# Kernel tuning notes

Measured on AMD Instinct MI355X. Metric: run time of the kernel, lower is better.

Reference implementation:

```python
import jax, jax.numpy as jnp
import numpy as np

# Production-scale dims (see shape_source)
B, H, W, C = 8, 64, 64, 256
KH, KW = 3, 3
BASES = 16
FILTERS = 256


def setup_inputs() -> dict:
    key = jax.random.key(0)
    k1, k2, k3, k4 = jax.random.split(key, 4)
    x = jax.random.normal(k1, (B, H, W, C), dtype=jnp.float32)
    # P: channel-mixing matrix [C, C] (initialized to identity in build, then assigned)
    P = jax.random.normal(k2, (C, C), dtype=jnp.float32) * 0.05
    # Q: per-channel basis kernels [C, kh, kw, bases]
    Q = jax.random.normal(k3, (C, KH, KW, BASES), dtype=jnp.float32) * 0.1
    # S: basis-combination weights [C, bases, filters]
    S = jax.random.normal(k4, (C, BASES, FILTERS), dtype=jnp.float32) * 0.05
    return {"x": x, "P": P, "Q": Q, "S": S}


def reference(x, P, Q, S):
    # --- Step 1: channel mixing (the vectorized_map over calculate_J) ---
    # J[o] = sum_c x[..., c] * P[o, c]  ->  one GEMM over channels
    mixed = jnp.einsum('bhwc,oc->bhwo', x, P)  # [B,H,W,C]

    C_ = P.shape[0]
    kh, kw, bases = Q.shape[1], Q.shape[2], Q.shape[3]

    # --- Step 2: per-channel conv with `bases` basis kernels (the map_fn loop) ---
    # Expressed as ONE grouped (depthwise-style) conv: group c produces outputs
    # [c*bases : (c+1)*bases], matching kernel flatten order (c, b).
    rhs = jnp.transpose(Q, (1, 2, 0, 3)).reshape(kh, kw, 1, C_ * bases)  # HWIO
    dw = jax.lax.conv_general_dilated(
        mixed, rhs, window_strides=(1, 1), padding='VALID',
        dimension_numbers=('NHWC', 'HWIO', 'NHWC'),
        feature_group_count=C_,
    )  # [B, H-kh+1, W-kw+1, C*bases], channel index k = c*bases + b

    b, h, w, _ = dw.shape
    # tau in the original: [B, h, w, bases, C]
    tau = dw.reshape(b, h, w, C_, bases).transpose(0, 1, 2, 4, 3)

    # --- Step 3: basis-weighted combination (the vectorized_map over calculate_O) ---
    # Original flattens tau row-major over (bases, C) and S[:, :, f] row-major over
    # (C, bases), then does an elementwise dot over the flat axis. Replicate exactly.
    Tflat = tau.reshape(b, h, w, bases * C_)          # flat index k = b_idx*C + c
    Sflat = S.reshape(C_ * bases, S.shape[-1])        # flat index k = c*bases + b_idx
    O = jnp.einsum('bhwk,kf->bhwf', Tflat, Sflat)     # [B, h, w, filters]
    return O
```

## Files before the change

### kernel.cpp

```cpp
#include <hip/hip_runtime.h>
#include <hip/hip_bf16.h>

typedef __attribute__((ext_vector_type(4))) float f32x4;
typedef __attribute__((ext_vector_type(8))) short bf16x8;

#define M_TOT 30752

__device__ __forceinline__ unsigned short f2bf(float f) {
  unsigned int u = __float_as_uint(f);
  u = u + 0x7FFF + ((u >> 16) & 1);
  return (unsigned short)(u >> 16);
}

__device__ __forceinline__ void gload16(const void* g, void* l) {
  __builtin_amdgcn_global_load_lds((const __attribute__((address_space(1))) unsigned int*)g,
                                   (__attribute__((address_space(3))) unsigned int*)l,
                                   16, 0, 0);
}

__global__ __launch_bounds__(256) void prep1(const float* __restrict__ x,
                                             const float* __restrict__ Q,
                                             const float* __restrict__ S,
                                             unsigned short* __restrict__ xb,
                                             float* __restrict__ Keff) {
  const int bid = blockIdx.x;
  const int t = threadIdx.x;

  if (bid < 4096) {
    int i = bid * 256 + t;
    const f32x4* xp = (const f32x4*)x;
    f32x4 a = xp[2 * i];
    f32x4 b = xp[2 * i + 1];
    bf16x8 o;
    o[0] = (short)f2bf(a[0]); o[1] = (short)f2bf(a[1]);
    o[2] = (short)f2bf(a[2]); o[3] = (short)f2bf(a[3]);
    o[4] = (short)f2bf(b[0]); o[5] = (short)f2bf(b[1]);
    o[6] = (short)f2bf(b[2]); o[7] = (short)f2bf(b[3]);
    ((bf16x8*)xb)[i] = o;
    return;
  }

  const int bid2 = bid - 4096;
  const int o = bid2 / 9;
  const int kk = bid2 - o * 9;
  const int f = t;
  const int qb = o * 144 + kk * 16;
  const int sb = (o >> 4) * 4096 + (o & 15) * 256 + f;
  float acc = 0.f;
#pragma unroll
  for (int bi = 0; bi < 16; ++bi)
    acc = fmaf(Q[qb + bi], S[sb + bi * 65536], acc);
  Keff[bid2 * 256 + f] = acc;
}

__global__ __launch_bounds__(256) void k2t_k(const float* __restrict__ P,
                                             const float* __restrict__ Keff,
                                             unsigned short* __restrict__ K2t) {
  const int kk = blockIdx.x >> 6;
  const int f0 = (blockIdx.x & 63) * 4;
  const int ci = threadIdx.x;
  float acc[4] = {0.f, 0.f, 0.f, 0.f};
#pragma unroll 8
  for (int o = 0; o < 256; ++o) {
    float pv = P[o * 256 + ci];
    const float* ke = Keff + (o * 9 + kk) * 256 + f0;
    acc[0] = fmaf(pv, ke[0], acc[0]);
    acc[1] = fmaf(pv, ke[1], acc[1]);
    acc[2] = fmaf(pv, ke[2], acc[2]);
    acc[3] = fmaf(pv, ke[3], acc[3]);
  }
#pragma unroll
  for (int j = 0; j < 4; ++j)
    K2t[kk * 65536 + (f0 + j) * 256 + ci] = f2bf(acc[j]);
}

__global__ __launch_bounds__(512) void conv_gemm(const unsigned short* __restrict__ xb,
                                                 const unsigned short* __restrict__ K2t,
                                                 float* __restrict__ out) {
  __shared__ unsigned short A0[128 * 64];
  __shared__ unsigned short A1[128 * 64];
  __shared__ unsigned short A2[128 * 64];
  __shared__ unsigned short B0[256 * 64];
  __shared__ unsigned short B1[256 * 64];
  __shared__ unsigned short B2[256 * 64];

  const int tid = threadIdx.x;
  const int lane = tid & 63;
  const int wm = (tid >> 6) >> 2;
  const int wn = (tid >> 6) & 3;
  const int m0 = blockIdx.x * 128;

  const int swslot = ((tid & 7) ^ ((tid >> 3) & 7)) * 8;
  const int rA = tid >> 3;

  int gA0, gA1;
  {
    int m = m0 + rA; if (m >= M_TOT) m = M_TOT - 1;
    int b = m / 3844; int rem = m - b * 3844;
    int h = rem / 62; int w = rem - h * 62;
    gA0 = ((b * 64 + h) * 64 + w) * 256 + swslot;
    m = m0 + rA + 64; if (m >= M_TOT) m = M_TOT - 1;
    b = m / 3844; rem = m - b * 3844;
    h = rem / 62; w = rem - h * 62;
    gA1 = ((b * 64 + h) * 64 + w) * 256 + swslot;
  }

  f32x4 zero = {0.f, 0.f, 0.f, 0.f};
  f32x4 acc[4][4];
#pragma unroll
  for (int i = 0; i < 4; ++i)
#pragma unroll
    for (int j = 0; j < 4; ++j) acc[i][j] = zero;

  const int rl = lane & 15;
  const int kg = lane >> 4;
  const int xm = (lane & 7) << 4;

#define STAGE_A(t, bufA)                                                       \
  {                                                                            \
    int kk_ = (t) >> 2, cb_ = (t) & 3;                                         \
    int kh_ = kk_ / 3, kw_ = kk_ - kh_ * 3;                                    \
    int offA_ = kh_ * 16384 + kw_ * 256 + cb_ * 64;                            \
    gload16(xb + gA0 + offA_, &bufA[tid * 8]);                                 \
    gload16(xb + gA1 + offA_, &bufA[(tid + 512) * 8]);                         \
  }

#define STAGE_B(t, bufB)                                                       \
  {                                                                            \
    int kk_ = (t) >> 2, cb_ = (t) & 3;                                         \
    int offB_ = kk_ * 65536 + cb_ * 64 + swslot;                               \
    _Pragma("unroll")                                                          \
    for (int q = 0; q < 4; ++q)                                                \
      gload16(K2t + offB_ + (rA + 64 * q) * 256, &bufB[(tid + 512 * q) * 8]);  \
  }

#define PHASE(ks, bufA, bufB, STAGE_STMT)                                      \
  {                                                                            \
    bf16x8 af[4], bfr[4];                                                      \
    int cbyte = ((ks) * 64 + kg * 16) ^ xm;                                    \
    _Pragma("unroll")                                                          \
    for (int mi = 0; mi < 4; ++mi)                                             \
      af[mi] = *(const bf16x8*)((const char*)bufA + (wm * 64 + mi * 16 + rl) * 128 + cbyte); \
    _Pragma("unroll")                                                          \
    for (int ni = 0; ni < 4; ++ni)                                             \
      bfr[ni] = *(const bf16x8*)((const char*)bufB + (wn * 64 + ni * 16 + rl) * 128 + cbyte); \
    STAGE_STMT;                                                                \
    asm volatile("s_waitcnt lgkmcnt(0)" ::: "memory");                         \
    __builtin_amdgcn_sched_barrier(0);                                         \
    __builtin_amdgcn_s_setprio(1);                                             \
    _Pragma("unroll")                                                          \
    for (int mi = 0; mi < 4; ++mi)                                             \
      _Pragma("unroll")                                                        \
      for (int ni = 0; ni < 4; ++ni)                                           \
        acc[mi][ni] = __builtin_amdgcn_mfma_f32_16x16x32_bf16(                 \
            af[mi], bfr[ni], acc[mi][ni], 0, 0, 0);                            \
    __builtin_amdgcn_s_setprio(0);                                             \
  }

#define STEP(t, cA, cB, nA, nB)                                                \
  {                                                                            \
    if ((t) == 35) asm volatile("s_waitcnt vmcnt(0)" ::: "memory");            \
    else           asm volatile("s_waitcnt vmcnt(6)" ::: "memory");            \
    __builtin_amdgcn_sched_barrier(0);                                         \
    __builtin_amdgcn_s_barrier();                                              \
    __builtin_amdgcn_sched_barrier(0);                                         \
    PHASE(0, cA, cB, { if ((t) + 2 < 36) STAGE_A((t) + 2, nA); })              \
    __builtin_amdgcn_sched_barrier(0);                                         \
    __builtin_amdgcn_s_barrier();                                              \
    __builtin_amdgcn_sched_barrier(0);                                         \
    PHASE(1, cA, cB, { if ((t) + 2 < 36) STAGE_B((t) + 2, nB); })              \
  }

  STAGE_A(0, A0); STAGE_B(0, B0);
  STAGE_A(1, A1); STAGE_B(1, B1);

  for (int tt = 0; tt < 12; ++tt) {
    int t0 = tt * 3;
    STEP(t0,     A0, B0, A2, B2);
    STEP(t0 + 1, A1, B1, A0, B0);
    STEP(t0 + 2, A2, B2, A1, B1);
  }

#pragma unroll
  for (int mi = 0; mi < 4; ++mi) {
    int mb = m0 + wm * 64 + mi * 16 + kg * 4;
#pragma unroll
    for (int ni = 0; ni < 4; ++ni) {
      int f = wn * 64 + ni * 16 + rl;
#pragma unroll
      for (int r = 0; r < 4; ++r) {
        int m = mb + r;
        if (m < M_TOT) out[m * 256 + f] = acc[mi][ni][r];
      }
    }
  }
#undef STAGE_A
#undef STAGE_B
#undef PHASE
#undef STEP
}

extern "C" void kernel_launch(void* const* d_in, const int* in_sizes, int n_in,
                              void* d_out, int out_size, void* d_ws, size_t ws_size,
                              hipStream_t stream) {
  const float* x = (const float*)d_in[0];
  const float* P = (const float*)d_in[1];
  const float* Q = (const float*)d_in[2];
  const float* S = (const float*)d_in[3];
  float* out = (float*)d_out;

  char* ws = (char*)d_ws;
  unsigned short* xb   = (unsigned short*)ws;
  unsigned short* K2t  = (unsigned short*)(ws + 16777216);
  float*          Keff = (float*)(ws + 16777216 + 1179648);

  prep1<<<4096 + 2304, 256, 0, stream>>>(x, Q, S, xb, Keff);
  k2t_k<<<576, 256, 0, stream>>>(P, Keff, K2t);
  conv_gemm<<<241, 512, 0, stream>>>(xb, K2t, out);
}
```

Baseline: 80.27 us.

## Split-K across warp halves in conv GEMM with LDS reduction; reuse S loads in prep

The conv GEMM now splits each 64-wide K chunk between two groups of 4 waves. Each wave computes a full 128-row by 64-column tile (8x4 MFMAs) over half of K, and the two halves are reduced through LDS at the end. The per-K-step two-phase barrier structure collapses into one phase per step. LDS staging is reworked into a single 144KB buffer without the XOR swizzle, which risks bank conflicts, and accumulator registers double. The Keff prep kernel loads the 16 S values once per channel and reuses them across all 9 taps, cutting its block count from 2304 to 256.

Result: faster. 77.76 us (-3.1%).

```diff
diff --git a/kernel.cpp b/kernel.cpp
--- a/kernel.cpp
+++ b/kernel.cpp
@@ -40,17 +40,19 @@
     return;
   }
 
-  const int bid2 = bid - 4096;
-  const int o = bid2 / 9;
-  const int kk = bid2 - o * 9;
-  const int f = t;
-  const int qb = o * 144 + kk * 16;
-  const int sb = (o >> 4) * 4096 + (o & 15) * 256 + f;
-  float acc = 0.f;
-#pragma unroll
-  for (int bi = 0; bi < 16; ++bi)
-    acc = fmaf(Q[qb + bi], S[sb + bi * 65536], acc);
-  Keff[bid2 * 256 + f] = acc;
+  const int o = bid - 4096;
+  float s[16];
+  const float* sp = S + (o >> 4) * 4096 + (o & 15) * 256 + t;
+#pragma unroll
+  for (int bi = 0; bi < 16; ++bi) s[bi] = sp[bi * 65536];
+  const float* qp = Q + o * 144;
+#pragma unroll
+  for (int kk = 0; kk < 9; ++kk) {
+    float a = 0.f;
+#pragma unroll
+    for (int bi = 0; bi < 16; ++bi) a = fmaf(qp[kk * 16 + bi], s[bi], a);
+    Keff[(o * 9 + kk) * 256 + t] = a;
+  }
 }
 
 __global__ __launch_bounds__(256) void k2t_k(const float* __restrict__ P,
@@ -74,87 +76,59 @@
     K2t[kk * 65536 + (f0 + j) * 256 + ci] = f2bf(acc[j]);
 }
 
-__global__ __launch_bounds__(512) void conv_gemm(const unsigned short* __restrict__ xb,
-                                                 const unsigned short* __restrict__ K2t,
-                                                 float* __restrict__ out) {
-  __shared__ unsigned short A0[128 * 64];
-  __shared__ unsigned short A1[128 * 64];
-  __shared__ unsigned short A2[128 * 64];
-  __shared__ unsigned short B0[256 * 64];
-  __shared__ unsigned short B1[256 * 64];
-  __shared__ unsigned short B2[256 * 64];
+__global__ __launch_bounds__(512, 2) void conv_gemm(const unsigned short* __restrict__ xb,
+                                                    const unsigned short* __restrict__ K2t,
+                                                    float* __restrict__ out) {
+  __shared__ __attribute__((aligned(16))) char smem[147456];
+  unsigned short* const A0 = (unsigned short*)(smem);
+  unsigned short* const B0 = (unsigned short*)(smem + 16384);
+  unsigned short* const A1 = (unsigned short*)(smem + 49152);
+  unsigned short* const B1 = (unsigned short*)(smem + 65536);
+  unsigned short* const A2 = (unsigned short*)(smem + 98304);
+  unsigned short* const B2 = (unsigned short*)(smem + 114688);
+  float* const red = (float*)smem;
 
   const int tid = threadIdx.x;
   const int lane = tid & 63;
-  const int wm = (tid >> 6) >> 2;
+  const int sk = tid >> 8;
   const int wn = (tid >> 6) & 3;
   const int m0 = blockIdx.x * 128;
 
-  const int swslot = ((tid & 7) ^ ((tid >> 3) & 7)) * 8;
-  const int rA = tid >> 3;
-
-  int gA0, gA1;
+  const int rl = lane & 15;
+  const int kg = lane >> 4;
+
+  int gAa;
   {
-    int m = m0 + rA; if (m >= M_TOT) m = M_TOT - 1;
+    int m = m0 + (tid >> 2); if (m >= M_TOT) m = M_TOT - 1;
     int b = m / 3844; int rem = m - b * 3844;
     int h = rem / 62; int w = rem - h * 62;
-    gA0 = ((b * 64 + h) * 64 + w) * 256 + swslot;
-    m = m0 + rA + 64; if (m >= M_TOT) m = M_TOT - 1;
-    b = m / 3844; rem = m - b * 3844;
-    h = rem / 62; w = rem - h * 62;
-    gA1 = ((b * 64 + h) * 64 + w) * 256 + swslot;
-  }
+    gAa = ((b * 64 + h) * 64 + w) * 256 + (tid & 3) * 8;
+  }
+  const int fB0 = (tid >> 2) * 256 + (tid & 3) * 8;
+  const int fB1 = ((tid >> 2) + 128) * 256 + (tid & 3) * 8;
 
   f32x4 zero = {0.f, 0.f, 0.f, 0.f};
-  f32x4 acc[4][4];
-#pragma unroll
-  for (int i = 0; i < 4; ++i)
+  f32x4 acc[8][4];
+#pragma unroll
+  for (int i = 0; i < 8; ++i)
 #pragma unroll
     for (int j = 0; j < 4; ++j) acc[i][j] = zero;
 
-  const int rl = lane & 15;
-  const int kg = lane >> 4;
-  const int xm = (lane & 7) << 4;
-
-#define STAGE_A(t, bufA)                                                       \
+  const int aoff = sk * 8192 + rl * 64 + kg * 16;
+  const int boff = sk * 16384 + (wn * 64 + rl) * 64 + kg * 16;
+
+#define STAGE(t, bufA, bufB)                                                   \
   {                                                                            \
     int kk_ = (t) >> 2, cb_ = (t) & 3;                                         \
     int kh_ = kk_ / 3, kw_ = kk_ - kh_ * 3;                                    \
     int offA_ = kh_ * 16384 + kw_ * 256 + cb_ * 64;                            \
-    gload16(xb + gA0 + offA_, &bufA[tid * 8]);                                 \
-    gload16(xb + gA1 + offA_, &bufA[(tid + 512) * 8]);                         \
-  }
-
-#define STAGE_B(t, bufB)                                                       \
-  {                                                                            \
-    int kk_ = (t) >> 2, cb_ = (t) & 3;                                         \
-    int offB_ = kk_ * 65536 + cb_ * 64 + swslot;                               \
-    _Pragma("unroll")                                                          \
-    for (int q = 0; q < 4; ++q)                                                \
-      gload16(K2t + offB_ + (rA + 64 * q) * 256, &bufB[(tid + 512 * q) * 8]);  \
-  }
-
-#define PHASE(ks, bufA, bufB, STAGE_STMT)                                      \
-  {                                                                            \
-    bf16x8 af[4], bfr[4];                                                      \
-    int cbyte = ((ks) * 64 + kg * 16) ^ xm;                                    \
-    _Pragma("unroll")                                                          \
-    for (int mi = 0; mi < 4; ++mi)                                             \
-      af[mi] = *(const bf16x8*)((const char*)bufA + (wm * 64 + mi * 16 + rl) * 128 + cbyte); \
-    _Pragma("unroll")                                                          \
-    for (int ni = 0; ni < 4; ++ni)                                             \
-      bfr[ni] = *(const bf16x8*)((const char*)bufB + (wn * 64 + ni * 16 + rl) * 128 + cbyte); \
-    STAGE_STMT;                                                                \
-    asm volatile("s_waitcnt lgkmcnt(0)" ::: "memory");                         \
-    __builtin_amdgcn_sched_barrier(0);                                         \
-    __builtin_amdgcn_s_setprio(1);                                             \
-    _Pragma("unroll")                                                          \
-    for (int mi = 0; mi < 4; ++mi)                                             \
-      _Pragma("unroll")                                                        \
-      for (int ni = 0; ni < 4; ++ni)                                           \
-        acc[mi][ni] = __builtin_amdgcn_mfma_f32_16x16x32_bf16(                 \
-            af[mi], bfr[ni], acc[mi][ni], 0, 0, 0);                            \
-    __builtin_amdgcn_s_setprio(0);                                             \
+    int offB_ = kk_ * 65536 + cb_ * 64;                                        \
+    gload16(xb + gAa + offA_,       &bufA[tid * 8]);                           \
+    gload16(xb + gAa + offA_ + 32,  &bufA[(tid + 512) * 8]);                   \
+    gload16(K2t + offB_ + fB0,      &bufB[tid * 8]);                           \
+    gload16(K2t + offB_ + fB1,      &bufB[(tid + 512) * 8]);                   \
+    gload16(K2t + offB_ + fB0 + 32, &bufB[(tid + 1024) * 8]);                  \
+    gload16(K2t + offB_ + fB1 + 32, &bufB[(tid + 1536) * 8]);                  \
   }
 
 #define STEP(t, cA, cB, nA, nB)                                                \
@@ -164,15 +138,28 @@
     __builtin_amdgcn_sched_barrier(0);                                         \
     __builtin_amdgcn_s_barrier();                                              \
     __builtin_amdgcn_sched_barrier(0);                                         \
-    PHASE(0, cA, cB, { if ((t) + 2 < 36) STAGE_A((t) + 2, nA); })              \
+    bf16x8 af[8], bfr[4];                                                      \
+    _Pragma("unroll")                                                          \
+    for (int mi = 0; mi < 8; ++mi)                                             \
+      af[mi] = *(const bf16x8*)((const char*)(cA) + aoff + mi * 1024);         \
+    _Pragma("unroll")                                                          \
+    for (int ni = 0; ni < 4; ++ni)                                             \
+      bfr[ni] = *(const bf16x8*)((const char*)(cB) + boff + ni * 1024);        \
+    if ((t) < 34) { STAGE((t) + 2, nA, nB); }                                  \
+    asm volatile("s_waitcnt lgkmcnt(0)" ::: "memory");                         \
     __builtin_amdgcn_sched_barrier(0);                                         \
-    __builtin_amdgcn_s_barrier();                                              \
-    __builtin_amdgcn_sched_barrier(0);                                         \
-    PHASE(1, cA, cB, { if ((t) + 2 < 36) STAGE_B((t) + 2, nB); })              \
-  }
-
-  STAGE_A(0, A0); STAGE_B(0, B0);
-  STAGE_A(1, A1); STAGE_B(1, B1);
+    __builtin_amdgcn_s_setprio(1);                                             \
+    _Pragma("unroll")                                                          \
+    for (int mi = 0; mi < 8; ++mi)                                             \
+      _Pragma("unroll")                                                        \
+      for (int ni = 0; ni < 4; ++ni)                                           \
+        acc[mi][ni] = __builtin_amdgcn_mfma_f32_16x16x32_bf16(                 \
+            af[mi], bfr[ni], acc[mi][ni], 0, 0, 0);                            \
+    __builtin_amdgcn_s_setprio(0);                                             \
+  }
+
+  STAGE(0, A0, B0);
+  STAGE(1, A1, B1);
 
   for (int tt = 0; tt < 12; ++tt) {
     int t0 = tt * 3;
@@ -181,22 +168,40 @@
     STEP(t0 + 2, A2, B2, A1, B1);
   }
 
-#pragma unroll
-  for (int mi = 0; mi < 4; ++mi) {
-    int mb = m0 + wm * 64 + mi * 16 + kg * 4;
-#pragma unroll
-    for (int ni = 0; ni < 4; ++ni) {
-      int f = wn * 64 + ni * 16 + rl;
-#pragma unroll
-      for (int r = 0; r < 4; ++r) {
-        int m = mb + r;
-        if (m < M_TOT) out[m * 256 + f] = acc[mi][ni][r];
+  __syncthreads();
+
+#pragma unroll
+  for (int round = 0; round < 2; ++round) {
+    if (sk == 1) {
+#pragma unroll
+      for (int mc = 0; mc < 4; ++mc)
+#pragma unroll
+        for (int ni = 0; ni < 4; ++ni)
+          *(f32x4*)((char*)red + (((wn * 4 + mc) * 4 + ni) * 64 + lane) * 16) =
+              acc[round * 4 + mc][ni];
+    }
+    __syncthreads();
+    if (sk == 0) {
+#pragma unroll
+      for (int mc = 0; mc < 4; ++mc) {
+        int mi = round * 4 + mc;
+        int mb = m0 + mi * 16 + kg * 4;
+#pragma unroll
+        for (int ni = 0; ni < 4; ++ni) {
+          f32x4 o = *(f32x4*)((char*)red + (((wn * 4 + mc) * 4 + ni) * 64 + lane) * 16);
+          o += acc[mi][ni];
+          int f = wn * 64 + ni * 16 + rl;
+#pragma unroll
+          for (int r = 0; r < 4; ++r) {
+            int m = mb + r;
+            if (m < M_TOT) out[m * 256 + f] = o[r];
+          }
+        }
       }
     }
-  }
-#undef STAGE_A
-#undef STAGE_B
-#undef PHASE
+    __syncthreads();
+  }
+#undef STAGE
 #undef STEP
 }
 
@@ -214,7 +219,7 @@
   unsigned short* K2t  = (unsigned short*)(ws + 16777216);
   float*          Keff = (float*)(ws + 16777216 + 1179648);
 
-  prep1<<<4096 + 2304, 256, 0, stream>>>(x, Q, S, xb, Keff);
+  prep1<<<4096 + 256, 256, 0, stream>>>(x, Q, S, xb, Keff);
   k2t_k<<<576, 256, 0, stream>>>(P, Keff, K2t);
   conv_gemm<<<241, 512, 0, stream>>>(xb, K2t, out);
 }
```

## Fuse weight-prep kernels and split GEMM phases into finer MFMA/load interleave

Applied to the files above, without the earlier changes.

Merges the Keff and K2t preparation into a single kernel that launches alongside the x-to-bf16 conversion. Each block recomputes its Keff slice into LDS, so the Keff round trip through global memory and one launch are gone, at the cost of some redundant Q·S work. The conv GEMM now keeps A and B in one contiguous LDS buffer per stage. Each K step is split into four 8-MFMA chunks with the B prefetch spread across them, aiming to overlap global loads with compute more evenly. The price is extra barriers per step.

After: 77.92 us. 2.9% less time.

```diff
diff --git a/kernel.cpp b/kernel.cpp
--- a/kernel.cpp
+++ b/kernel.cpp
@@ -18,16 +18,18 @@
                                    16, 0, 0);
 }
 
-__global__ __launch_bounds__(256) void prep1(const float* __restrict__ x,
-                                             const float* __restrict__ Q,
-                                             const float* __restrict__ S,
-                                             unsigned short* __restrict__ xb,
-                                             float* __restrict__ Keff) {
+__global__ __launch_bounds__(256) void fused_k(const float* __restrict__ x,
+                                               const float* __restrict__ P,
+                                               const float* __restrict__ Q,
+                                               const float* __restrict__ S,
+                                               unsigned short* __restrict__ xb,
+                                               unsigned short* __restrict__ K2t) {
+  __shared__ float ldsK[256 * 4];
   const int bid = blockIdx.x;
   const int t = threadIdx.x;
 
-  if (bid < 4096) {
-    int i = bid * 256 + t;
+  if (bid >= 576) {
+    int i = (bid - 576) * 256 + t;
     const f32x4* xp = (const f32x4*)x;
     f32x4 a = xp[2 * i];
     f32x4 b = xp[2 * i + 1];
@@ -40,49 +42,44 @@
     return;
   }
 
-  const int bid2 = bid - 4096;
-  const int o = bid2 / 9;
-  const int kk = bid2 - o * 9;
-  const int f = t;
-  const int qb = o * 144 + kk * 16;
-  const int sb = (o >> 4) * 4096 + (o & 15) * 256 + f;
-  float acc = 0.f;
-#pragma unroll
-  for (int bi = 0; bi < 16; ++bi)
-    acc = fmaf(Q[qb + bi], S[sb + bi * 65536], acc);
-  Keff[bid2 * 256 + f] = acc;
-}
-
-__global__ __launch_bounds__(256) void k2t_k(const float* __restrict__ P,
-                                             const float* __restrict__ Keff,
-                                             unsigned short* __restrict__ K2t) {
-  const int kk = blockIdx.x >> 6;
-  const int f0 = (blockIdx.x & 63) * 4;
-  const int ci = threadIdx.x;
-  float acc[4] = {0.f, 0.f, 0.f, 0.f};
+  const int kk = bid / 64;
+  const int f0 = (bid & 63) * 4;
+  {
+    float k0 = 0.f, k1 = 0.f, k2 = 0.f, k3 = 0.f;
+    const float* qp = Q + t * 144 + kk * 16;
+    const float* sp = S + (t >> 4) * 4096 + (t & 15) * 256 + f0;
+#pragma unroll
+    for (int bi = 0; bi < 16; ++bi) {
+      float qv = qp[bi];
+      const float* s4 = sp + bi * 65536;
+      k0 = fmaf(qv, s4[0], k0); k1 = fmaf(qv, s4[1], k1);
+      k2 = fmaf(qv, s4[2], k2); k3 = fmaf(qv, s4[3], k3);
+    }
+    ldsK[t * 4 + 0] = k0; ldsK[t * 4 + 1] = k1;
+    ldsK[t * 4 + 2] = k2; ldsK[t * 4 + 3] = k3;
+  }
+  __syncthreads();
+  {
+    const int ci = t;
+    float acc[4] = {0.f, 0.f, 0.f, 0.f};
 #pragma unroll 8
-  for (int o = 0; o < 256; ++o) {
-    float pv = P[o * 256 + ci];
-    const float* ke = Keff + (o * 9 + kk) * 256 + f0;
-    acc[0] = fmaf(pv, ke[0], acc[0]);
-    acc[1] = fmaf(pv, ke[1], acc[1]);
-    acc[2] = fmaf(pv, ke[2], acc[2]);
-    acc[3] = fmaf(pv, ke[3], acc[3]);
-  }
-#pragma unroll
-  for (int j = 0; j < 4; ++j)
-    K2t[kk * 65536 + (f0 + j) * 256 + ci] = f2bf(acc[j]);
+    for (int o = 0; o < 256; ++o) {
+      float pv = P[o * 256 + ci];
+      acc[0] = fmaf(pv, ldsK[o * 4 + 0], acc[0]);
+      acc[1] = fmaf(pv, ldsK[o * 4 + 1], acc[1]);
+      acc[2] = fmaf(pv, ldsK[o * 4 + 2], acc[2]);
+      acc[3] = fmaf(pv, ldsK[o * 4 + 3], acc[3]);
+    }
+#pragma unroll
+    for (int j = 0; j < 4; ++j)
+      K2t[kk * 65536 + (f0 + j) * 256 + ci] = f2bf(acc[j]);
+  }
 }
 
 __global__ __launch_bounds__(512) void conv_gemm(const unsigned short* __restrict__ xb,
                                                  const unsigned short* __restrict__ K2t,
                                                  float* __restrict__ out) {
-  __shared__ unsigned short A0[128 * 64];
-  __shared__ unsigned short A1[128 * 64];
-  __shared__ unsigned short A2[128 * 64];
-  __shared__ unsigned short B0[256 * 64];
-  __shared__ unsigned short B1[256 * 64];
-  __shared__ unsigned short B2[256 * 64];
+  __shared__ __attribute__((aligned(16))) char smem[147456];
 
   const int tid = threadIdx.x;
   const int lane = tid & 63;
@@ -104,6 +101,9 @@
     h = rem / 62; w = rem - h * 62;
     gA1 = ((b * 64 + h) * 64 + w) * 256 + swslot;
   }
+  int fB[4];
+#pragma unroll
+  for (int q = 0; q < 4; ++q) fB[q] = (rA + 64 * q) * 256 + swslot;
 
   f32x4 zero = {0.f, 0.f, 0.f, 0.f};
   f32x4 acc[4][4];
@@ -116,69 +116,89 @@
   const int kg = lane >> 4;
   const int xm = (lane & 7) << 4;
 
-#define STAGE_A(t, bufA)                                                       \
+#define STAGE_A(t, base)                                                       \
   {                                                                            \
     int kk_ = (t) >> 2, cb_ = (t) & 3;                                         \
     int kh_ = kk_ / 3, kw_ = kk_ - kh_ * 3;                                    \
     int offA_ = kh_ * 16384 + kw_ * 256 + cb_ * 64;                            \
-    gload16(xb + gA0 + offA_, &bufA[tid * 8]);                                 \
-    gload16(xb + gA1 + offA_, &bufA[(tid + 512) * 8]);                         \
-  }
-
-#define STAGE_B(t, bufB)                                                       \
+    unsigned short* bA = (unsigned short*)(base);                              \
+    gload16(xb + gA0 + offA_, bA + tid * 8);                                   \
+    gload16(xb + gA1 + offA_, bA + (tid + 512) * 8);                           \
+  }
+#define STAGE_B2(t, base, q0)                                                  \
   {                                                                            \
     int kk_ = (t) >> 2, cb_ = (t) & 3;                                         \
-    int offB_ = kk_ * 65536 + cb_ * 64 + swslot;                               \
-    _Pragma("unroll")                                                          \
-    for (int q = 0; q < 4; ++q)                                                \
-      gload16(K2t + offB_ + (rA + 64 * q) * 256, &bufB[(tid + 512 * q) * 8]);  \
-  }
-
-#define PHASE(ks, bufA, bufB, STAGE_STMT)                                      \
-  {                                                                            \
-    bf16x8 af[4], bfr[4];                                                      \
-    int cbyte = ((ks) * 64 + kg * 16) ^ xm;                                    \
-    _Pragma("unroll")                                                          \
-    for (int mi = 0; mi < 4; ++mi)                                             \
-      af[mi] = *(const bf16x8*)((const char*)bufA + (wm * 64 + mi * 16 + rl) * 128 + cbyte); \
-    _Pragma("unroll")                                                          \
-    for (int ni = 0; ni < 4; ++ni)                                             \
-      bfr[ni] = *(const bf16x8*)((const char*)bufB + (wn * 64 + ni * 16 + rl) * 128 + cbyte); \
-    STAGE_STMT;                                                                \
+    int offB_ = kk_ * 65536 + cb_ * 64;                                        \
+    unsigned short* bB = (unsigned short*)((char*)(base) + 16384);             \
+    gload16(K2t + offB_ + fB[q0],     bB + (tid + 512 * (q0)) * 8);            \
+    gload16(K2t + offB_ + fB[q0 + 1], bB + (tid + 512 * (q0 + 1)) * 8);        \
+  }
+
+#define AF(mi, ks, buf) \
+  (*(const bf16x8*)((const char*)(buf) + (wm * 64 + (mi) * 16 + rl) * 128 + (((ks) * 64 + kg * 16) ^ xm)))
+#define BF(ni, ks, buf) \
+  (*(const bf16x8*)((const char*)(buf) + 16384 + (wn * 64 + (ni) * 16 + rl) * 128 + (((ks) * 64 + kg * 16) ^ xm)))
+
+#define FENCE_MFMA8(M0, M1, b0, b1, b2, b3, a0_, a1_)                          \
+  {                                                                            \
+    __builtin_amdgcn_sched_barrier(0);                                         \
+    __builtin_amdgcn_s_barrier();                                              \
     asm volatile("s_waitcnt lgkmcnt(0)" ::: "memory");                         \
     __builtin_amdgcn_sched_barrier(0);                                         \
     __builtin_amdgcn_s_setprio(1);                                             \
-    _Pragma("unroll")                                                          \
-    for (int mi = 0; mi < 4; ++mi)                                             \
-      _Pragma("unroll")                                                        \
-      for (int ni = 0; ni < 4; ++ni)                                           \
-        acc[mi][ni] = __builtin_amdgcn_mfma_f32_16x16x32_bf16(                 \
-            af[mi], bfr[ni], acc[mi][ni], 0, 0, 0);                            \
+    acc[M0][0] = __builtin_amdgcn_mfma_f32_16x16x32_bf16(a0_, b0, acc[M0][0], 0, 0, 0); \
+    acc[M0][1] = __builtin_amdgcn_mfma_f32_16x16x32_bf16(a0_, b1, acc[M0][1], 0, 0, 0); \
+    acc[M0][2] = __builtin_amdgcn_mfma_f32_16x16x32_bf16(a0_, b2, acc[M0][2], 0, 0, 0); \
+    acc[M0][3] = __builtin_amdgcn_mfma_f32_16x16x32_bf16(a0_, b3, acc[M0][3], 0, 0, 0); \
+    acc[M1][0] = __builtin_amdgcn_mfma_f32_16x16x32_bf16(a1_, b0, acc[M1][0], 0, 0, 0); \
+    acc[M1][1] = __builtin_amdgcn_mfma_f32_16x16x32_bf16(a1_, b1, acc[M1][1], 0, 0, 0); \
+    acc[M1][2] = __builtin_amdgcn_mfma_f32_16x16x32_bf16(a1_, b2, acc[M1][2], 0, 0, 0); \
+    acc[M1][3] = __builtin_amdgcn_mfma_f32_16x16x32_bf16(a1_, b3, acc[M1][3], 0, 0, 0); \
     __builtin_amdgcn_s_setprio(0);                                             \
-  }
-
-#define STEP(t, cA, cB, nA, nB)                                                \
-  {                                                                            \
-    if ((t) == 35) asm volatile("s_waitcnt vmcnt(0)" ::: "memory");            \
+    __builtin_amdgcn_sched_barrier(0);                                         \
+    __builtin_amdgcn_s_barrier();                                              \
+    __builtin_amdgcn_sched_barrier(0);                                         \
+  }
+
+#define STEP(t, cur, nxt)                                                      \
+  {                                                                            \
+    if ((t) >= 34) asm volatile("s_waitcnt vmcnt(0)" ::: "memory");            \
     else           asm volatile("s_waitcnt vmcnt(6)" ::: "memory");            \
     __builtin_amdgcn_sched_barrier(0);                                         \
     __builtin_amdgcn_s_barrier();                                              \
     __builtin_amdgcn_sched_barrier(0);                                         \
-    PHASE(0, cA, cB, { if ((t) + 2 < 36) STAGE_A((t) + 2, nA); })              \
-    __builtin_amdgcn_sched_barrier(0);                                         \
-    __builtin_amdgcn_s_barrier();                                              \
-    __builtin_amdgcn_sched_barrier(0);                                         \
-    PHASE(1, cA, cB, { if ((t) + 2 < 36) STAGE_B((t) + 2, nB); })              \
-  }
-
-  STAGE_A(0, A0); STAGE_B(0, B0);
-  STAGE_A(1, A1); STAGE_B(1, B1);
+    bf16x8 b0, b1, b2, b3, a0, a1;                                             \
+                \
+    b0 = BF(0, 0, cur); b1 = BF(1, 0, cur); b2 = BF(2, 0, cur); b3 = BF(3, 0, cur); \
+    a0 = AF(0, 0, cur); a1 = AF(1, 0, cur);                                    \
+    if ((t) + 2 < 36) STAGE_A((t) + 2, nxt);                                   \
+    FENCE_MFMA8(0, 1, b0, b1, b2, b3, a0, a1)                                  \
+                              \
+    a0 = AF(2, 0, cur); a1 = AF(3, 0, cur);                                    \
+    if ((t) + 2 < 36) STAGE_B2((t) + 2, nxt, 0);                               \
+    FENCE_MFMA8(2, 3, b0, b1, b2, b3, a0, a1)                                  \
+                     \
+    b0 = BF(0, 1, cur); b1 = BF(1, 1, cur); b2 = BF(2, 1, cur); b3 = BF(3, 1, cur); \
+    a0 = AF(0, 1, cur); a1 = AF(1, 1, cur);                                    \
+    if ((t) + 2 < 36) STAGE_B2((t) + 2, nxt, 2);                               \
+    FENCE_MFMA8(0, 1, b0, b1, b2, b3, a0, a1)                                  \
+                              \
+    a0 = AF(2, 1, cur); a1 = AF(3, 1, cur);                                    \
+    FENCE_MFMA8(2, 3, b0, b1, b2, b3, a0, a1)                                  \
+  }
+
+  char* B0 = smem;
+  char* B1 = smem + 49152;
+  char* B2 = smem + 98304;
+
+  STAGE_A(0, B0); STAGE_B2(0, B0, 0); STAGE_B2(0, B0, 2);
+  STAGE_A(1, B1); STAGE_B2(1, B1, 0); STAGE_B2(1, B1, 2);
 
   for (int tt = 0; tt < 12; ++tt) {
     int t0 = tt * 3;
-    STEP(t0,     A0, B0, A2, B2);
-    STEP(t0 + 1, A1, B1, A0, B0);
-    STEP(t0 + 2, A2, B2, A1, B1);
+    STEP(t0,     B0, B2);
+    STEP(t0 + 1, B1, B0);
+    STEP(t0 + 2, B2, B1);
   }
 
 #pragma unroll
@@ -195,8 +215,10 @@
     }
   }
 #undef STAGE_A
-#undef STAGE_B
-#undef PHASE
+#undef STAGE_B2
+#undef AF
+#undef BF
+#undef FENCE_MFMA8
 #undef STEP
 }
 
@@ -210,11 +232,9 @@
   float* out = (float*)d_out;
 
   char* ws = (char*)d_ws;
-  unsigned short* xb   = (unsigned short*)ws;
-  unsigned short* K2t  = (unsigned short*)(ws + 16777216);
-  float*          Keff = (float*)(ws + 16777216 + 1179648);
-
-  prep1<<<4096 + 2304, 256, 0, stream>>>(x, Q, S, xb, Keff);
-  k2t_k<<<576, 256, 0, stream>>>(P, Keff, K2t);
+  unsigned short* xb  = (unsigned short*)ws;
+  unsigned short* K2t = (unsigned short*)(ws + 16777216);
+
+  fused_k<<<4672, 256, 0, stream>>>(x, P, Q, S, xb, K2t);
   conv_gemm<<<241, 512, 0, stream>>>(xb, K2t, out);
 }
```
